# Optimization experiments

Measured on AMD Instinct MI355X. Metric: run time of the kernel, lower is better.

Reference implementation:

```python
import jax, jax.numpy as jnp
import numpy as np

B, NN, BBX, CLS, LAT = 8192, 64, 6, 16, 128
IN = LAT + NN + CLS  # 208
NT = B * NN          # total nodes in batched graph
NE = 4_194_304       # random edges (avg degree 8)


def setup_inputs() -> dict:
    key = jax.random.key(0)
    ks = jax.random.split(key, 16)
    p = lambda i, sh: (jax.random.normal(ks[i], sh, dtype=jnp.float32) * 0.05)
    return {
        "embedding": jax.random.normal(ks[0], (B, IN), dtype=jnp.float32),
        "E": jax.random.randint(ks[1], (2, NE), 0, NT, dtype=jnp.int32),
        "refine_iter": 2,
        "W1": p(2, (IN, 128)), "b1": p(3, (128,)),
        "W2": p(4, (128, 128)), "b2": p(5, (128,)),
        "Wbbx": p(6, (128, NN * BBX)), "bbbx": p(7, (NN * BBX,)),
        "Wlbl": p(8, (128, NN)), "blbl": p(9, (NN,)),
        "Wedge": p(10, (128, NN * NN)), "bedge": p(11, (NN * NN,)),
        "Wcls": p(12, (128, CLS)), "bcls": p(13, (CLS,)),
        "Wg": p(14, (BBX, BBX)), "bg": p(15, (BBX,)),
    }


def _gcn(h, src, dst, Wg, bg):
    # PyG GCNConv with add_self_loops=True, bias: D^-1/2 (A+I) D^-1/2 (h W) + b
    deg = jax.ops.segment_sum(jnp.ones(src.shape, h.dtype), dst, num_segments=NT)
    dinv = jax.lax.rsqrt(deg)  # deg >= 1 thanks to self-loops
    norm = dinv[src] * dinv[dst]
    m = h @ Wg  # [NT, BBX]
    out = jax.ops.segment_sum(m[src] * norm[:, None], dst, num_segments=NT)
    return out + bg


def reference(embedding, E, refine_iter, W1, b1, W2, b2, Wbbx, bbbx,
              Wlbl, blbl, Wedge, bedge, Wcls, bcls, Wg, bg):
    sig = jax.nn.sigmoid
    x = sig(embedding @ W1 + b1)
    x = sig(x @ W2 + b2)
    x = sig(x @ W2 + b2)  # dense2 applied twice (shared weights), as in source
    x_bbx = sig(x @ Wbbx + bbbx).reshape(B, NN, BBX)
    x_lbl = sig(x @ Wlbl + blbl).reshape(B, NN, 1)
    x_edge = sig(x @ Wedge + bedge).reshape(B, NN, NN)
    class_pred = jax.nn.softmax(x @ Wcls + bcls, axis=-1)

    loops = jnp.arange(NT, dtype=E.dtype)
    src = jnp.concatenate([E[0], loops])
    dst = jnp.concatenate([E[1], loops])

    x_bbx_refined = x_bbx
    for _ in range(int(refine_iter)):
        x_masked = x_bbx_refined * x_lbl  # labels=None -> mask with x_lbl
        flat = x_masked.reshape(NT, BBX)
        corr = jax.nn.sigmoid(_gcn(flat, src, dst, Wg, bg))
        # NOTE: source adds correction to the MASKED features (faithful)
        x_bbx_refined = (flat + corr).reshape(B, NN, BBX)
    return (x_bbx, x_lbl, x_edge, class_pred, x_bbx_refined)
```

## Files before the change

kernel.cpp:

```cpp
#include <hip/hip_runtime.h>
#include <hip/hip_bf16.h>
#include <math.h>

#define B_      8192
#define IN_     208
#define INP_    224
#define H_      128
#define NN_     64
#define BBX_    6
#define CLS_    16
#define NT_     (B_*NN_)
#define NE_     4194304
#define NB_     256
#define BSH_    11
#define CH_     8192
#define CAP_    18432

typedef __attribute__((ext_vector_type(8))) short short8v;
typedef __attribute__((ext_vector_type(4))) float f32x4;
typedef __attribute__((ext_vector_type(2))) float f32x2;

__device__ __forceinline__ float sigmoidf_(float v){ return 1.0f/(1.0f+__expf(-v)); }
__device__ __forceinline__ unsigned f2bf_(float f){
  unsigned u = __float_as_uint(f);
  return (u + 0x7FFFu + ((u >> 16) & 1u)) >> 16;
}

#if defined(__has_builtin)
# if __has_builtin(__builtin_amdgcn_cvt_pk_fp8_f32) && __has_builtin(__builtin_amdgcn_cvt_pk_f32_fp8)
#  define HW_FP8 1
# endif
#endif
#ifndef HW_FP8
# define HW_FP8 0
#endif

#if !HW_FP8
__device__ __forceinline__ unsigned enc1_(float v){
  unsigned u = __float_as_uint(v);
  unsigned s = (u >> 31) << 7;
  unsigned a = u & 0x7FFFFFFFu;
  unsigned r8;
  if (a < 0x3D000000u) {
    int q = (int)rintf(__uint_as_float(a) * 512.0f);
    r8 = (unsigned)q;
  } else {
    unsigned r = a + 0x7FFFFu + ((a >> 20) & 1u);
    int eb = (int)(r >> 23) - 120;
    r8 = (eb > 15) ? 0x7Eu : (unsigned)((eb << 3) | ((r >> 20) & 7u));
  }
  return s | r8;
}
__device__ __forceinline__ float dec1_(unsigned b){
  unsigned m = b & 7u, e = (b >> 3) & 0xFu;
  float mag = e ? __uint_as_float(((e + 120u) << 23) | (m << 20))
               : (float)m * 0.001953125f;
  return (b & 0x80u) ? -mag : mag;
}
#endif

__device__ __forceinline__ uint2 enc6_(const float mm[6]){
  uint2 o;
#if HW_FP8
  int w0 = __builtin_amdgcn_cvt_pk_fp8_f32(mm[0], mm[1], 0, false);
  w0     = __builtin_amdgcn_cvt_pk_fp8_f32(mm[2], mm[3], w0, true);
  int w1 = __builtin_amdgcn_cvt_pk_fp8_f32(mm[4], mm[5], 0, false);
  o.x = (unsigned)w0; o.y = (unsigned)w1;
#else
  o.x = enc1_(mm[0]) | (enc1_(mm[1])<<8) | (enc1_(mm[2])<<16) | (enc1_(mm[3])<<24);
  o.y = enc1_(mm[4]) | (enc1_(mm[5])<<8);
#endif
  return o;
}
__device__ __forceinline__ void dec6_(uint2 w, float v[6]){
#if HW_FP8
  f32x2 a = __builtin_amdgcn_cvt_pk_f32_fp8(w.x, false);
  f32x2 b = __builtin_amdgcn_cvt_pk_f32_fp8(w.x, true);
  f32x2 c = __builtin_amdgcn_cvt_pk_f32_fp8(w.y, false);
  v[0]=a[0]; v[1]=a[1]; v[2]=b[0]; v[3]=b[1]; v[4]=c[0]; v[5]=c[1];
#else
  v[0]=dec1_(w.x & 255u); v[1]=dec1_((w.x>>8)&255u);
  v[2]=dec1_((w.x>>16)&255u); v[3]=dec1_(w.x>>24);
  v[4]=dec1_(w.y & 255u); v[5]=dec1_((w.y>>8)&255u);
#endif
}

__global__ __launch_bounds__(256) void gemm_bias_act(
    const float* __restrict__ A, const float* __restrict__ W,
    const float* __restrict__ bias, float* __restrict__ C,
    int M, int N, int K, int act)
{
  __shared__ float As[16][64];
  __shared__ float Bs[16][64];
  const int tid = threadIdx.x;
  const int bm = blockIdx.y * 64;
  const int bn = blockIdx.x * 64;
  const int tx = tid & 15;
  const int ty = tid >> 4;
  const int arow = tid >> 2;
  const int acol = (tid & 3) << 2;
  const int brow = tid >> 4;
  const int bcol = (tid & 15) << 2;

  float acc[4][4] = {};

  for (int k0 = 0; k0 < K; k0 += 16) {
    float4 av = *reinterpret_cast<const float4*>(A + (size_t)(bm + arow) * K + k0 + acol);
    float4 bv = *reinterpret_cast<const float4*>(W + (size_t)(k0 + brow) * N + bn + bcol);
    __syncthreads();
    As[acol+0][arow] = av.x; As[acol+1][arow] = av.y;
    As[acol+2][arow] = av.z; As[acol+3][arow] = av.w;
    *reinterpret_cast<float4*>(&Bs[brow][bcol]) = bv;
    __syncthreads();
    #pragma unroll
    for (int k = 0; k < 16; ++k) {
      float4 a = *reinterpret_cast<const float4*>(&As[k][ty << 2]);
      float4 b = *reinterpret_cast<const float4*>(&Bs[k][tx << 2]);
      float ar[4] = {a.x, a.y, a.z, a.w};
      float br[4] = {b.x, b.y, b.z, b.w};
      #pragma unroll
      for (int i = 0; i < 4; ++i)
        #pragma unroll
        for (int j = 0; j < 4; ++j)
          acc[i][j] = fmaf(ar[i], br[j], acc[i][j]);
    }
  }

  #pragma unroll
  for (int i = 0; i < 4; ++i) {
    const int row = bm + (ty << 2) + i;
    float4 o;
    float* op = &o.x;
    #pragma unroll
    for (int j = 0; j < 4; ++j) {
      float v = acc[i][j] + bias[bn + (tx << 2) + j];
      op[j] = act ? sigmoidf_(v) : v;
    }
    *reinterpret_cast<float4*>(C + (size_t)row * N + bn + (tx << 2)) = o;
  }
}

__global__ __launch_bounds__(256) void cast_emb_k(const float* __restrict__ emb,
                                                  unsigned short* __restrict__ Eb) {
  const int i = blockIdx.x * 256 + threadIdx.x;
  const int row = i / (INP_/8), c = (i % (INP_/8)) * 8;
  ushort4 lo = {0,0,0,0}, hi = {0,0,0,0};
  if (c < IN_) {
    const float* src = emb + (size_t)row * IN_ + c;
    float4 v0 = *reinterpret_cast<const float4*>(src);
    float4 v1 = *reinterpret_cast<const float4*>(src + 4);
    lo.x=(unsigned short)f2bf_(v0.x); lo.y=(unsigned short)f2bf_(v0.y);
    lo.z=(unsigned short)f2bf_(v0.z); lo.w=(unsigned short)f2bf_(v0.w);
    hi.x=(unsigned short)f2bf_(v1.x); hi.y=(unsigned short)f2bf_(v1.y);
    hi.z=(unsigned short)f2bf_(v1.z); hi.w=(unsigned short)f2bf_(v1.w);
  }
  ushort4* dst = reinterpret_cast<ushort4*>(Eb + (size_t)row * INP_ + c);
  dst[0] = lo; dst[1] = hi;
}

__global__ __launch_bounds__(256) void transpose_w1_k(const float* __restrict__ W,
                                                      unsigned short* __restrict__ Wt) {
  const int i = blockIdx.x * 256 + threadIdx.x;
  if (i >= H_ * INP_) return;
  const int n = i / INP_, k = i % INP_;
  Wt[i] = (k < IN_) ? (unsigned short)f2bf_(W[(size_t)k * H_ + n]) : 0;
}

__global__ __launch_bounds__(256) void transpose_all_k(
    const float* __restrict__ We, unsigned short* __restrict__ WtE,
    const float* __restrict__ Wb, unsigned short* __restrict__ WtB,
    const float* __restrict__ W2, unsigned short* __restrict__ Wt2) {
  __shared__ unsigned short tile[64][136];
  const int t = threadIdx.x;
  const float* W; unsigned short* Wt; int N, n0;
  if (blockIdx.x < 64)      { W = We; Wt = WtE; N = 4096; n0 = blockIdx.x * 64; }
  else if (blockIdx.x < 70) { W = Wb; Wt = WtB; N = 384;  n0 = (blockIdx.x-64) * 64; }
  else                      { W = W2; Wt = Wt2; N = 128;  n0 = (blockIdx.x-70) * 64; }
  const int kk = t >> 6;
  const int nn = t & 63;
  for (int k0 = 0; k0 < 128; k0 += 4)
    tile[nn][k0 + kk] = (unsigned short)f2bf_(W[(size_t)(k0 + kk) * N + n0 + nn]);
  __syncthreads();
  const int rr = t >> 2, c0 = (t & 3) * 32;
  ushort4* dst = reinterpret_cast<ushort4*>(Wt + (size_t)(n0 + rr) * 128 + c0);
  #pragma unroll
  for (int q = 0; q < 8; ++q) {
    ushort4 o;
    o.x = tile[rr][c0 + q*4 + 0]; o.y = tile[rr][c0 + q*4 + 1];
    o.z = tile[rr][c0 + q*4 + 2]; o.w = tile[rr][c0 + q*4 + 3];
    dst[q] = o;
  }
}

__global__ __launch_bounds__(256) void gemm_mfma_trunk(
    const unsigned short* __restrict__ Ab,
    const unsigned short* __restrict__ Wt,
    const float* __restrict__ bias,
    unsigned short* __restrict__ Cb,
    float* __restrict__ Cf,
    int Kp)
{
  const int tid  = threadIdx.x;
  const int wave = tid >> 6, lane = tid & 63;
  const int wm = wave >> 1, wn = wave & 1;
  const int r = lane & 15, g = lane >> 4;
  const int rowA0 = blockIdx.y * 128 + wm * 64;
  const int colB0 = wn * 64;

  f32x4 acc[4][4];
  #pragma unroll
  for (int i = 0; i < 4; ++i)
    #pragma unroll
    for (int j = 0; j < 4; ++j)
      acc[i][j] = (f32x4){0.f, 0.f, 0.f, 0.f};

  for (int ks = 0; ks < Kp / 32; ++ks) {
    const int koff = ks * 32 + g * 8;
    short8v a[4], b[4];
    #pragma unroll
    for (int i = 0; i < 4; ++i)
      a[i] = *reinterpret_cast<const short8v*>(Ab + (size_t)(rowA0 + i*16 + r) * Kp + koff);
    #pragma unroll
    for (int j = 0; j < 4; ++j)
      b[j] = *reinterpret_cast<const short8v*>(Wt + (size_t)(colB0 + j*16 + r) * Kp + koff);
    #pragma unroll
    for (int i = 0; i < 4; ++i)
      #pragma unroll
      for (int j = 0; j < 4; ++j)
        acc[i][j] = __builtin_amdgcn_mfma_f32_16x16x32_bf16(a[i], b[j], acc[i][j], 0, 0, 0);
  }

  #pragma unroll
  for (int j = 0; j < 4; ++j) {
    const int col = colB0 + j*16 + r;
    const float bc = bias[col];
    #pragma unroll
    for (int i = 0; i < 4; ++i) {
      const int row0 = rowA0 + i*16 + g*4;
      #pragma unroll
      for (int q = 0; q < 4; ++q) {
        const float v = sigmoidf_(acc[i][j][q] + bc);
        if (Cb) Cb[(size_t)(row0 + q) * H_ + col] = (unsigned short)f2bf_(v);
        if (Cf) Cf[(size_t)(row0 + q) * H_ + col] = v;
      }
    }
  }
}

__global__ __launch_bounds__(256) void gemm_mfma_head(
    const unsigned short* __restrict__ Xb,
    const unsigned short* __restrict__ Wt,
    const float* __restrict__ bias, float* __restrict__ C, int N)
{
  const int tid  = threadIdx.x;
  const int wave = tid >> 6, lane = tid & 63;
  const int wm = wave >> 1, wn = wave & 1;
  const int r = lane & 15, g = lane >> 4;
  const int rowA0 = blockIdx.y * 128 + wm * 64;
  const int colB0 = blockIdx.x * 128 + wn * 64;

  f32x4 acc[4][4];
  #pragma unroll
  for (int i = 0; i < 4; ++i)
    #pragma unroll
    for (int j = 0; j < 4; ++j)
      acc[i][j] = (f32x4){0.f, 0.f, 0.f, 0.f};

  #pragma unroll
  for (int ks = 0; ks < 4; ++ks) {
    const int koff = ks * 32 + g * 8;
    short8v a[4], b[4];
    #pragma unroll
    for (int i = 0; i < 4; ++i)
      a[i] = *reinterpret_cast<const short8v*>(Xb + (size_t)(rowA0 + i*16 + r) * 128 + koff);
    #pragma unroll
    for (int j = 0; j < 4; ++j)
      b[j] = *reinterpret_cast<const short8v*>(Wt + (size_t)(colB0 + j*16 + r) * 128 + koff);
    #pragma unroll
    for (int i = 0; i < 4; ++i)
      #pragma unroll
      for (int j = 0; j < 4; ++j)
        acc[i][j] = __builtin_amdgcn_mfma_f32_16x16x32_bf16(a[i], b[j], acc[i][j], 0, 0, 0);
  }

  #pragma unroll
  for (int j = 0; j < 4; ++j) {
    const int col = colB0 + j*16 + r;
    const float bc = bias[col];
    #pragma unroll
    for (int i = 0; i < 4; ++i) {
      const int row0 = rowA0 + i*16 + g*4;
      #pragma unroll
      for (int q = 0; q < 4; ++q)
        C[(size_t)(row0 + q) * N + col] = sigmoidf_(acc[i][j][q] + bc);
    }
  }
}

__global__ __launch_bounds__(64) void cls_softmax_k(
    const float* __restrict__ X, const float* __restrict__ Wc,
    const float* __restrict__ bc, float* __restrict__ out)
{
  const int tid = threadIdx.x;
  const int r = blockIdx.x * 4 + (tid >> 4);
  const int c = tid & 15;
  const float* xr = X + (size_t)r * H_;
  float acc = bc[c];
  #pragma unroll 8
  for (int k = 0; k < H_; ++k) acc = fmaf(xr[k], Wc[k * CLS_ + c], acc);
  float mx = acc;
  for (int off = 8; off; off >>= 1) mx = fmaxf(mx, __shfl_xor(mx, off, 16));
  float e = __expf(acc - mx);
  float s = e;
  for (int off = 8; off; off >>= 1) s += __shfl_xor(s, off, 16);
  out[(size_t)r * CLS_ + c] = e / s;
}

__global__ __launch_bounds__(256) void binA_k(const int* __restrict__ E,
                                              int* __restrict__ gcnt,
                                              unsigned* __restrict__ binned) {
  __shared__ unsigned stage[CH_];
  __shared__ unsigned char stb[CH_];
  __shared__ int hist[NB_], lbase[NB_], gbase[NB_];
  const int t = threadIdx.x;
  const int e0 = blockIdx.x * CH_;

  hist[t] = 0;
  __syncthreads();

  unsigned pk[32];
  int rb[32];
  #pragma unroll
  for (int i = 0; i < 32; ++i) {
    const int e = e0 + i * 256 + t;
    const int s = E[e];
    const unsigned d = (unsigned)E[NE_ + e];
    const int b = d >> BSH_;
    pk[i] = (unsigned)s | ((d & 2047u) << 19);
    rb[i] = atomicAdd(&hist[b], 1) | (b << 20);
  }
  __syncthreads();

  const int v = hist[t];
  lbase[t] = v; __syncthreads();
  #pragma unroll
  for (int off = 1; off < NB_; off <<= 1) {
    int x = (t >= off) ? lbase[t - off] : 0;
    __syncthreads();
    lbase[t] += x;
    __syncthreads();
  }
  const int excl = lbase[t] - v;
  __syncthreads();
  lbase[t] = excl;
  gbase[t] = t * CAP_ + atomicAdd(&gcnt[t], v);
  __syncthreads();

  #pragma unroll
  for (int i = 0; i < 32; ++i) {
    const int b = rb[i] >> 20;
    const int pos = lbase[b] + (rb[i] & 0xFFFFF);
    stage[pos] = pk[i];
    stb[pos] = (unsigned char)b;
  }
  __syncthreads();

  for (int i = t; i < CH_; i += 256) {
    const int b = stb[i];
    const int tgt = gbase[b] + (i - lbase[b]);
    if (tgt < (b + 1) * CAP_)
      binned[tgt] = stage[i];
  }
}

__global__ __launch_bounds__(1024) void csr_k(const int* __restrict__ gcnt,
                                              const unsigned* __restrict__ binned,
                                              int* __restrict__ rowptr, int* __restrict__ cnt_g,
                                              float* __restrict__ dinv, int* __restrict__ csr_src) {
  __shared__ int cnt[2048];
  __shared__ int sd[1024];
  const int t = threadIdx.x, b = blockIdx.x;
  const int beg = b * CAP_;
  const int end = beg + min(gcnt[b], CAP_);

  cnt[t] = 0; cnt[t + 1024] = 0;
  __syncthreads();
  for (int i = beg + t; i < end; i += 1024)
    atomicAdd(&cnt[binned[i] >> 19], 1);
  __syncthreads();

  const int c0 = cnt[2 * t], c1 = cnt[2 * t + 1];
  const int s = c0 + c1;
  sd[t] = s; __syncthreads();
  #pragma unroll
  for (int off = 1; off < 1024; off <<= 1) {
    int x = (t >= off) ? sd[t - off] : 0;
    __syncthreads();
    sd[t] += x;
    __syncthreads();
  }
  const int excl = sd[t] - s;

  const int node0 = b * 2048 + 2 * t;
  rowptr[node0]     = beg + excl;
  rowptr[node0 + 1] = beg + excl + c0;
  cnt_g[node0]      = c0;
  cnt_g[node0 + 1]  = c1;
  dinv[node0]       = rsqrtf(1.0f + (float)c0);
  dinv[node0 + 1]   = rsqrtf(1.0f + (float)c1);
  __syncthreads();
  cnt[2 * t] = excl;
  cnt[2 * t + 1] = excl + c0;
  __syncthreads();

  for (int i = beg + t; i < end; i += 1024) {
    const unsigned pk = binned[i];
    const int dl = pk >> 19;
    const int slot = atomicAdd(&cnt[dl], 1);
    csr_src[beg + slot] = (int)(pk & 0x7FFFFu);
  }
}

__global__ __launch_bounds__(256) void gcn_pre_k(
    const float* __restrict__ refined, const float* __restrict__ lbl,
    const float* __restrict__ Wg, const float* __restrict__ dinv,
    uint2* __restrict__ ms8)
{
  int i = blockIdx.x * 256 + threadIdx.x;
  if (i >= NT_) return;
  float l = lbl[i];
  float di = dinv[i];
  float f[6];
  #pragma unroll
  for (int j = 0; j < 6; ++j) f[j] = refined[(size_t)i * 6 + j] * l;
  float mm[6];
  #pragma unroll
  for (int j = 0; j < 6; ++j) {
    float acc = 0.f;
    #pragma unroll
    for (int k = 0; k < 6; ++k) acc = fmaf(f[k], Wg[k * 6 + j], acc);
    mm[j] = acc * di;
  }
  ms8[i] = enc6_(mm);
}

template<int WRITE_MS>
__global__ __launch_bounds__(256) void gcn_gather_k(
    const float* __restrict__ rin, float* __restrict__ rout,
    const float* __restrict__ lbl,
    const uint2* __restrict__ ms8_in, uint2* __restrict__ ms8_out,
    const float* __restrict__ dinv,
    const int* __restrict__ rowptr, const int* __restrict__ cnt,
    const int* __restrict__ csr_src, const float* __restrict__ bg,
    const float* __restrict__ Wg)
{
  int i = blockIdx.x * 256 + threadIdx.x;
  if (i >= NT_) return;
  const float di = dinv[i];
  const float l  = lbl[i];
  const int beg = rowptr[i];
  const int kend = beg + cnt[i];

  float acc[6];
  dec6_(ms8_in[i], acc);

  int k = beg;
  for (; k + 3 < kend; k += 4) {
    const int s0 = csr_src[k],   s1 = csr_src[k+1];
    const int s2 = csr_src[k+2], s3 = csr_src[k+3];
    const uint2 w0 = ms8_in[s0], w1 = ms8_in[s1];
    const uint2 w2 = ms8_in[s2], w3 = ms8_in[s3];
    float v0[6], v1[6], v2[6], v3[6];
    dec6_(w0, v0); dec6_(w1, v1); dec6_(w2, v2); dec6_(w3, v3);
    #pragma unroll
    for (int j = 0; j < 6; ++j) acc[j] += (v0[j] + v1[j]) + (v2[j] + v3[j]);
  }
  for (; k < kend; ++k) {
    float v[6];
    dec6_(ms8_in[csr_src[k]], v);
    #pragma unroll
    for (int j = 0; j < 6; ++j) acc[j] += v[j];
  }

  float nr[6];
  #pragma unroll
  for (int j = 0; j < 6; ++j) {
    const float flat = rin[(size_t)i * 6 + j] * l;
    nr[j] = flat + sigmoidf_(di * acc[j] + bg[j]);
    rout[(size_t)i * 6 + j] = nr[j];
  }

  if (WRITE_MS) {
    float f[6], mm[6];
    #pragma unroll
    for (int j = 0; j < 6; ++j) f[j] = nr[j] * l;
    #pragma unroll
    for (int j = 0; j < 6; ++j) {
      float a = 0.f;
      #pragma unroll
      for (int kk = 0; kk < 6; ++kk) a = fmaf(f[kk], Wg[kk * 6 + j], a);
      mm[j] = a * di;
    }
    ms8_out[i] = enc6_(mm);
  }
}

extern "C" void kernel_launch(void* const* d_in, const int* in_sizes, int n_in,
                              void* d_out, int out_size, void* d_ws, size_t ws_size,
                              hipStream_t stream)
{
  const float* emb   = (const float*)d_in[0];
  const int*   E     = (const int*)  d_in[1];
  const float* W1    = (const float*)d_in[3];
  const float* b1    = (const float*)d_in[4];
  const float* W2    = (const float*)d_in[5];
  const float* b2    = (const float*)d_in[6];
  const float* Wbbx  = (const float*)d_in[7];
  const float* bbbx  = (const float*)d_in[8];
  const float* Wlbl  = (const float*)d_in[9];
  const float* blbl  = (const float*)d_in[10];
  const float* Wedge = (const float*)d_in[11];
  const float* bedge = (const float*)d_in[12];
  const float* Wcls  = (const float*)d_in[13];
  const float* bcls  = (const float*)d_in[14];
  const float* Wg    = (const float*)d_in[15];
  const float* bg    = (const float*)d_in[16];

  float* out    = (float*)d_out;
  float* o_bbx  = out;
  float* o_lbl  = out + 3145728;
  float* o_edge = out + 3670016;
  float* o_cls  = out + 37224448;
  float* o_ref  = out + 37355520;

  char* wsb = (char*)d_ws;
  float* xB      = (float*)wsb;
  float* dinv    = xB + (size_t)B_ * H_;
  int*   cnt_g   = (int*)(dinv + NT_);
  int*   rowptr  = cnt_g + NT_;
  int*   csr_src = rowptr + NT_;
  char*  U       = (char*)(csr_src + (size_t)NB_ * CAP_);
  unsigned*       binned = (unsigned*)U;
  unsigned short* Eb   = (unsigned short*)U;
  unsigned short* x1b  = Eb  + (size_t)B_ * INP_;
  unsigned short* x2b  = x1b + (size_t)B_ * H_;
  unsigned short* Xb   = x2b + (size_t)B_ * H_;
  unsigned short* W1t  = Xb  + (size_t)B_ * H_;
  unsigned short* W2t  = W1t + (size_t)H_ * INP_;
  unsigned short* Wt_e = W2t + (size_t)H_ * H_;
  unsigned short* Wt_b = Wt_e + (size_t)4096 * H_;
  uint2*          ms8A = (uint2*)(Wt_b + (size_t)384 * H_);
  uint2*          ms8B = ms8A + NT_;
  int*            gcnt = (int*)(ms8B + NT_);

  hipMemsetAsync(gcnt, 0, NB_ * sizeof(int), stream);
  binA_k<<<NE_/CH_, 256, 0, stream>>>(E, gcnt, binned);
  csr_k <<<NB_, 1024, 0, stream>>>(gcnt, binned, rowptr, cnt_g, dinv, csr_src);

  cast_emb_k     <<<B_*(INP_/8)/256, 256, 0, stream>>>(emb, Eb);
  transpose_w1_k <<<(H_*INP_+255)/256, 256, 0, stream>>>(W1, W1t);
  transpose_all_k<<<72, 256, 0, stream>>>(Wedge, Wt_e, Wbbx, Wt_b, W2, W2t);

  gemm_mfma_trunk<<<dim3(1, B_/128), 256, 0, stream>>>(Eb,  W1t, b1, x1b, nullptr, INP_);
  gemm_mfma_trunk<<<dim3(1, B_/128), 256, 0, stream>>>(x1b, W2t, b2, x2b, nullptr, H_);
  gemm_mfma_trunk<<<dim3(1, B_/128), 256, 0, stream>>>(x2b, W2t, b2, Xb,  xB,      H_);

  gemm_mfma_head<<<dim3(4096/128, B_/128), 256, 0, stream>>>(Xb, Wt_e, bedge, o_edge, 4096);
  gemm_mfma_head<<<dim3(384/128,  B_/128), 256, 0, stream>>>(Xb, Wt_b, bbbx,  o_bbx,  384);
  gemm_bias_act<<<dim3(64/64, B_/64), 256, 0, stream>>>(xB, Wlbl, blbl, o_lbl, B_, 64, 128, 1);
  cls_softmax_k<<<B_/4, 64, 0, stream>>>(xB, Wcls, bcls, o_cls);

  gcn_pre_k<<<NT_/256, 256, 0, stream>>>(o_bbx, o_lbl, Wg, dinv, ms8A);
  gcn_gather_k<1><<<NT_/256, 256, 0, stream>>>(o_bbx, o_ref, o_lbl, ms8A, ms8B,
                                               dinv, rowptr, cnt_g, csr_src, bg, Wg);
  gcn_gather_k<0><<<NT_/256, 256, 0, stream>>>(o_ref, o_ref, o_lbl, ms8B, nullptr,
                                               dinv, rowptr, cnt_g, csr_src, bg, Wg);
}
```

Before: 262.5 us.

## Fuse trunk MLP layers into one kernel, merge weight prep, tune binning and gather

The three trunk GEMMs and the embedding cast become a single kernel. It converts fp32 embeddings to bf16 inline and keeps the intermediate activations in shared memory, so the bf16 intermediates no longer make round trips through global memory. The W1 transpose is folded into the other weight-transpose kernel, which cuts launches. The edge-binning chunk is halved to create more blocks, and the GCN gather gains an 8-wide unrolled loop for more memory-level parallelism. The fused trunk launches only 64 blocks, which may underuse the GPU.

New measurement: 244.5 us. 6.9% less time.

```diff
diff --git a/kernel.cpp b/kernel.cpp
--- a/kernel.cpp
+++ b/kernel.cpp
@@ -13,7 +13,7 @@
 #define NE_     4194304
 #define NB_     256
 #define BSH_    11
-#define CH_     8192
+#define CH_     4096
 #define CAP_    18432
 
 typedef __attribute__((ext_vector_type(8))) short short8v;
@@ -140,38 +140,22 @@
   }
 }
 
-__global__ __launch_bounds__(256) void cast_emb_k(const float* __restrict__ emb,
-                                                  unsigned short* __restrict__ Eb) {
-  const int i = blockIdx.x * 256 + threadIdx.x;
-  const int row = i / (INP_/8), c = (i % (INP_/8)) * 8;
-  ushort4 lo = {0,0,0,0}, hi = {0,0,0,0};
-  if (c < IN_) {
-    const float* src = emb + (size_t)row * IN_ + c;
-    float4 v0 = *reinterpret_cast<const float4*>(src);
-    float4 v1 = *reinterpret_cast<const float4*>(src + 4);
-    lo.x=(unsigned short)f2bf_(v0.x); lo.y=(unsigned short)f2bf_(v0.y);
-    lo.z=(unsigned short)f2bf_(v0.z); lo.w=(unsigned short)f2bf_(v0.w);
-    hi.x=(unsigned short)f2bf_(v1.x); hi.y=(unsigned short)f2bf_(v1.y);
-    hi.z=(unsigned short)f2bf_(v1.z); hi.w=(unsigned short)f2bf_(v1.w);
-  }
-  ushort4* dst = reinterpret_cast<ushort4*>(Eb + (size_t)row * INP_ + c);
-  dst[0] = lo; dst[1] = hi;
-}
-
-__global__ __launch_bounds__(256) void transpose_w1_k(const float* __restrict__ W,
-                                                      unsigned short* __restrict__ Wt) {
-  const int i = blockIdx.x * 256 + threadIdx.x;
-  if (i >= H_ * INP_) return;
-  const int n = i / INP_, k = i % INP_;
-  Wt[i] = (k < IN_) ? (unsigned short)f2bf_(W[(size_t)k * H_ + n]) : 0;
-}
-
-__global__ __launch_bounds__(256) void transpose_all_k(
+__global__ __launch_bounds__(256) void prep_k(
     const float* __restrict__ We, unsigned short* __restrict__ WtE,
     const float* __restrict__ Wb, unsigned short* __restrict__ WtB,
-    const float* __restrict__ W2, unsigned short* __restrict__ Wt2) {
+    const float* __restrict__ W2, unsigned short* __restrict__ Wt2,
+    const float* __restrict__ W1, unsigned short* __restrict__ W1t)
+{
   __shared__ unsigned short tile[64][136];
   const int t = threadIdx.x;
+  if (blockIdx.x >= 72) {
+    const int i = (blockIdx.x - 72) * 256 + t;
+    if (i < H_ * INP_) {
+      const int n = i / INP_, k = i % INP_;
+      W1t[i] = (k < IN_) ? (unsigned short)f2bf_(W1[(size_t)k * H_ + n]) : 0;
+    }
+    return;
+  }
   const float* W; unsigned short* Wt; int N, n0;
   if (blockIdx.x < 64)      { W = We; Wt = WtE; N = 4096; n0 = blockIdx.x * 64; }
   else if (blockIdx.x < 70) { W = Wb; Wt = WtB; N = 384;  n0 = (blockIdx.x-64) * 64; }
@@ -192,56 +176,119 @@
   }
 }
 
-__global__ __launch_bounds__(256) void gemm_mfma_trunk(
-    const unsigned short* __restrict__ Ab,
-    const unsigned short* __restrict__ Wt,
-    const float* __restrict__ bias,
-    unsigned short* __restrict__ Cb,
-    float* __restrict__ Cf,
-    int Kp)
-{
+__global__ __launch_bounds__(256) void fused_trunk_k(
+    const float* __restrict__ emb,
+    const unsigned short* __restrict__ W1t,
+    const float* __restrict__ b1,
+    const unsigned short* __restrict__ W2t,
+    const float* __restrict__ b2,
+    unsigned short* __restrict__ Xb, float* __restrict__ xB)
+{
+  __shared__ unsigned short s[128][136];
   const int tid  = threadIdx.x;
   const int wave = tid >> 6, lane = tid & 63;
   const int wm = wave >> 1, wn = wave & 1;
   const int r = lane & 15, g = lane >> 4;
-  const int rowA0 = blockIdx.y * 128 + wm * 64;
   const int colB0 = wn * 64;
+  const int growA = blockIdx.x * 128 + wm * 64;
 
   f32x4 acc[4][4];
+  short8v a[4], b[4];
+
   #pragma unroll
   for (int i = 0; i < 4; ++i)
     #pragma unroll
     for (int j = 0; j < 4; ++j)
       acc[i][j] = (f32x4){0.f, 0.f, 0.f, 0.f};
 
-  for (int ks = 0; ks < Kp / 32; ++ks) {
+  for (int ks = 0; ks < INP_/32; ++ks) {
     const int koff = ks * 32 + g * 8;
-    short8v a[4], b[4];
-    #pragma unroll
-    for (int i = 0; i < 4; ++i)
-      a[i] = *reinterpret_cast<const short8v*>(Ab + (size_t)(rowA0 + i*16 + r) * Kp + koff);
+    #pragma unroll
+    for (int i = 0; i < 4; ++i) {
+      if (koff < IN_) {
+        const float* src = emb + (size_t)(growA + i*16 + r) * IN_ + koff;
+        float4 v0 = *reinterpret_cast<const float4*>(src);
+        float4 v1 = *reinterpret_cast<const float4*>(src + 4);
+        a[i][0]=(short)f2bf_(v0.x); a[i][1]=(short)f2bf_(v0.y);
+        a[i][2]=(short)f2bf_(v0.z); a[i][3]=(short)f2bf_(v0.w);
+        a[i][4]=(short)f2bf_(v1.x); a[i][5]=(short)f2bf_(v1.y);
+        a[i][6]=(short)f2bf_(v1.z); a[i][7]=(short)f2bf_(v1.w);
+      } else {
+        a[i] = (short8v){0,0,0,0,0,0,0,0};
+      }
+    }
     #pragma unroll
     for (int j = 0; j < 4; ++j)
-      b[j] = *reinterpret_cast<const short8v*>(Wt + (size_t)(colB0 + j*16 + r) * Kp + koff);
+      b[j] = *reinterpret_cast<const short8v*>(W1t + (size_t)(colB0 + j*16 + r) * INP_ + koff);
     #pragma unroll
     for (int i = 0; i < 4; ++i)
       #pragma unroll
       for (int j = 0; j < 4; ++j)
         acc[i][j] = __builtin_amdgcn_mfma_f32_16x16x32_bf16(a[i], b[j], acc[i][j], 0, 0, 0);
   }
-
   #pragma unroll
   for (int j = 0; j < 4; ++j) {
     const int col = colB0 + j*16 + r;
-    const float bc = bias[col];
-    #pragma unroll
-    for (int i = 0; i < 4; ++i) {
-      const int row0 = rowA0 + i*16 + g*4;
-      #pragma unroll
-      for (int q = 0; q < 4; ++q) {
-        const float v = sigmoidf_(acc[i][j][q] + bc);
-        if (Cb) Cb[(size_t)(row0 + q) * H_ + col] = (unsigned short)f2bf_(v);
-        if (Cf) Cf[(size_t)(row0 + q) * H_ + col] = v;
+    const float bc = b1[col];
+    #pragma unroll
+    for (int i = 0; i < 4; ++i)
+      #pragma unroll
+      for (int q = 0; q < 4; ++q)
+        s[wm*64 + i*16 + g*4 + q][col] = (unsigned short)f2bf_(sigmoidf_(acc[i][j][q] + bc));
+  }
+  __syncthreads();
+
+  for (int layer = 0; layer < 2; ++layer) {
+    #pragma unroll
+    for (int i = 0; i < 4; ++i)
+      #pragma unroll
+      for (int j = 0; j < 4; ++j)
+        acc[i][j] = (f32x4){0.f, 0.f, 0.f, 0.f};
+
+    #pragma unroll
+    for (int ks = 0; ks < 4; ++ks) {
+      const int koff = ks * 32 + g * 8;
+      #pragma unroll
+      for (int i = 0; i < 4; ++i)
+        a[i] = *reinterpret_cast<const short8v*>(&s[wm*64 + i*16 + r][koff]);
+      #pragma unroll
+      for (int j = 0; j < 4; ++j)
+        b[j] = *reinterpret_cast<const short8v*>(W2t + (size_t)(colB0 + j*16 + r) * H_ + koff);
+      #pragma unroll
+      for (int i = 0; i < 4; ++i)
+        #pragma unroll
+        for (int j = 0; j < 4; ++j)
+          acc[i][j] = __builtin_amdgcn_mfma_f32_16x16x32_bf16(a[i], b[j], acc[i][j], 0, 0, 0);
+    }
+    __syncthreads();
+
+    if (layer == 0) {
+      #pragma unroll
+      for (int j = 0; j < 4; ++j) {
+        const int col = colB0 + j*16 + r;
+        const float bc = b2[col];
+        #pragma unroll
+        for (int i = 0; i < 4; ++i)
+          #pragma unroll
+          for (int q = 0; q < 4; ++q)
+            s[wm*64 + i*16 + g*4 + q][col] = (unsigned short)f2bf_(sigmoidf_(acc[i][j][q] + bc));
+      }
+      __syncthreads();
+    } else {
+      #pragma unroll
+      for (int j = 0; j < 4; ++j) {
+        const int col = colB0 + j*16 + r;
+        const float bc = b2[col];
+        #pragma unroll
+        for (int i = 0; i < 4; ++i) {
+          const int grow = blockIdx.x*128 + wm*64 + i*16 + g*4;
+          #pragma unroll
+          for (int q = 0; q < 4; ++q) {
+            const float v = sigmoidf_(acc[i][j][q] + bc);
+            Xb[(size_t)(grow + q) * H_ + col] = (unsigned short)f2bf_(v);
+            xB[(size_t)(grow + q) * H_ + col] = v;
+          }
+        }
       }
     }
   }
@@ -328,10 +375,10 @@
   hist[t] = 0;
   __syncthreads();
 
-  unsigned pk[32];
-  int rb[32];
-  #pragma unroll
-  for (int i = 0; i < 32; ++i) {
+  unsigned pk[CH_/256];
+  int rb[CH_/256];
+  #pragma unroll
+  for (int i = 0; i < CH_/256; ++i) {
     const int e = e0 + i * 256 + t;
     const int s = E[e];
     const unsigned d = (unsigned)E[NE_ + e];
@@ -357,7 +404,7 @@
   __syncthreads();
 
   #pragma unroll
-  for (int i = 0; i < 32; ++i) {
+  for (int i = 0; i < CH_/256; ++i) {
     const int b = rb[i] >> 20;
     const int pos = lbase[b] + (rb[i] & 0xFFFFF);
     stage[pos] = pk[i];
@@ -465,6 +512,21 @@
   dec6_(ms8_in[i], acc);
 
   int k = beg;
+  for (; k + 7 < kend; k += 8) {
+    int s_[8];
+    uint2 w_[8];
+    #pragma unroll
+    for (int u = 0; u < 8; ++u) s_[u] = csr_src[k + u];
+    #pragma unroll
+    for (int u = 0; u < 8; ++u) w_[u] = ms8_in[s_[u]];
+    #pragma unroll
+    for (int u = 0; u < 8; ++u) {
+      float v[6];
+      dec6_(w_[u], v);
+      #pragma unroll
+      for (int j = 0; j < 6; ++j) acc[j] += v[j];
+    }
+  }
   for (; k + 3 < kend; k += 4) {
     const int s0 = csr_src[k],   s1 = csr_src[k+1];
     const int s2 = csr_src[k+2], s3 = csr_src[k+3];
@@ -541,29 +603,22 @@
   int*   csr_src = rowptr + NT_;
   char*  U       = (char*)(csr_src + (size_t)NB_ * CAP_);
   unsigned*       binned = (unsigned*)U;
-  unsigned short* Eb   = (unsigned short*)U;
-  unsigned short* x1b  = Eb  + (size_t)B_ * INP_;
-  unsigned short* x2b  = x1b + (size_t)B_ * H_;
-  unsigned short* Xb   = x2b + (size_t)B_ * H_;
+  unsigned short* Xb   = (unsigned short*)U;
   unsigned short* W1t  = Xb  + (size_t)B_ * H_;
   unsigned short* W2t  = W1t + (size_t)H_ * INP_;
   unsigned short* Wt_e = W2t + (size_t)H_ * H_;
   unsigned short* Wt_b = Wt_e + (size_t)4096 * H_;
   uint2*          ms8A = (uint2*)(Wt_b + (size_t)384 * H_);
   uint2*          ms8B = ms8A + NT_;
-  int*            gcnt = (int*)(ms8B + NT_);
+  int*            gcnt = (int*)(U + (size_t)NB_ * CAP_ * 4);
 
   hipMemsetAsync(gcnt, 0, NB_ * sizeof(int), stream);
   binA_k<<<NE_/CH_, 256, 0, stream>>>(E, gcnt, binned);
   csr_k <<<NB_, 1024, 0, stream>>>(gcnt, binned, rowptr, cnt_g, dinv, csr_src);
 
-  cast_emb_k     <<<B_*(INP_/8)/256, 256, 0, stream>>>(emb, Eb);
-  transpose_w1_k <<<(H_*INP_+255)/256, 256, 0, stream>>>(W1, W1t);
-  transpose_all_k<<<72, 256, 0, stream>>>(Wedge, Wt_e, Wbbx, Wt_b, W2, W2t);
-
-  gemm_mfma_trunk<<<dim3(1, B_/128), 256, 0, stream>>>(Eb,  W1t, b1, x1b, nullptr, INP_);
-  gemm_mfma_trunk<<<dim3(1, B_/128), 256, 0, stream>>>(x1b, W2t, b2, x2b, nullptr, H_);
-  gemm_mfma_trunk<<<dim3(1, B_/128), 256, 0, stream>>>(x2b, W2t, b2, Xb,  xB,      H_);
+  prep_k<<<72 + (H_*INP_+255)/256, 256, 0, stream>>>(Wedge, Wt_e, Wbbx, Wt_b, W2, W2t, W1, W1t);
+
+  fused_trunk_k<<<B_/128, 256, 0, stream>>>(emb, W1t, b1, W2t, b2, Xb, xB);
 
   gemm_mfma_head<<<dim3(4096/128, B_/128), 256, 0, stream>>>(Xb, Wt_e, bedge, o_edge, 4096);
   gemm_mfma_head<<<dim3(384/128,  B_/128), 256, 0, stream>>>(Xb, Wt_b, bbbx,  o_bbx,  384);
```
